# Performance work log

Measured on AMD Instinct MI355X. Metric: run time of the kernel, lower is better.

Reference implementation:

```python
import jax, jax.numpy as jnp
from jax import lax
import numpy as np

STRIDE = 16
PRE_NMS = 2000
POST_NMS = 300
NMS_THRESH = 0.7
MIN_SIZE = 16.0  # * img_scale (=1.0)
DN = ('NCHW', 'OIHW', 'NCHW')


def _anchor_base(base=16, ratios=(0.5, 1.0, 2.0), scales=(8, 16, 32)):
    py = px = base / 2.0
    ab = np.zeros((len(ratios) * len(scales), 4), np.float32)
    k = 0
    for r in ratios:
        for s in scales:
            h = base * s * np.sqrt(r)
            w = base * s * np.sqrt(1.0 / r)
            ab[k] = [py - h / 2, px - w / 2, py + h / 2, px + w / 2]
            k += 1
    return ab


def _all_anchors(H, W, img_h, img_w):
    base = _anchor_base()
    sy = np.arange(H, dtype=np.float32) * STRIDE
    sx = np.arange(W, dtype=np.float32) * STRIDE
    yy, xx = np.meshgrid(sy, sx, indexing='ij')
    shifts = np.stack([yy, xx, yy, xx], axis=-1).reshape(-1, 1, 4)
    anchors = (shifts + base[None]).reshape(-1, 4).astype(np.float32)  # (H*W*9, 4)
    valid = np.where((anchors[:, 0] >= 0) & (anchors[:, 1] >= 0) &
                     (anchors[:, 2] <= img_h) & (anchors[:, 3] <= img_w))[0]
    return anchors, valid


def _loc2bbox(anc, loc):
    # anc: (1,K,4), loc: (B,K,4); boxes as (y1,x1,y2,x2)
    h = anc[..., 2] - anc[..., 0]
    w = anc[..., 3] - anc[..., 1]
    cy = anc[..., 0] + 0.5 * h
    cx = anc[..., 1] + 0.5 * w
    ncy = loc[..., 0] * h + cy
    ncx = loc[..., 1] * w + cx
    nh = h * jnp.exp(loc[..., 2])
    nw = w * jnp.exp(loc[..., 3])
    return jnp.stack([ncy - 0.5 * nh, ncx - 0.5 * nw,
                      ncy + 0.5 * nh, ncx + 0.5 * nw], axis=-1)


def _nms(boxes, scores):
    # boxes: (N,4), scores: (N,) -> (POST_NMS,4) zero-padded rois
    areas = (boxes[:, 2] - boxes[:, 0]) * (boxes[:, 3] - boxes[:, 1])

    def step(s, _):
        i = jnp.argmax(s)
        ok = s[i] > -jnp.inf
        b = boxes[i]
        yy1 = jnp.maximum(b[0], boxes[:, 0])
        xx1 = jnp.maximum(b[1], boxes[:, 1])
        yy2 = jnp.minimum(b[2], boxes[:, 2])
        xx2 = jnp.minimum(b[3], boxes[:, 3])
        inter = jnp.maximum(yy2 - yy1, 0.0) * jnp.maximum(xx2 - xx1, 0.0)
        iou = inter / (areas[i] + areas - inter + 1e-9)
        s = jnp.where(iou > NMS_THRESH, -jnp.inf, s).at[i].set(-jnp.inf)
        return s, (i, ok)

    _, (idx, ok) = lax.scan(step, scores, None, length=POST_NMS)
    return boxes[idx] * ok[:, None].astype(boxes.dtype)


def _conv(x, w, b, padding):
    y = lax.conv_general_dilated(x, w, (1, 1), padding, dimension_numbers=DN)
    return y + b[None, :, None, None]


def setup_inputs():
    key = jax.random.key(0)
    k = jax.random.split(key, 4)
    B, C, H, W = 2, 512, 64, 64
    std = 0.01
    return {
        'feat': jax.random.normal(k[0], (B, C, H, W), jnp.float32),
        'share_w': jax.random.normal(k[1], (512, 512, 3, 3), jnp.float32) * std,
        'share_b': jnp.zeros((512,), jnp.float32),
        'cls_w': jax.random.normal(k[2], (18, 512, 1, 1), jnp.float32) * std,
        'cls_b': jnp.zeros((18,), jnp.float32),
        'reg_w': jax.random.normal(k[3], (36, 512, 1, 1), jnp.float32) * std,
        'reg_b': jnp.zeros((36,), jnp.float32),
        'img_h': 1024,
        'img_w': 1024,
    }


def reference(feat, share_w, share_b, cls_w, cls_b, reg_w, reg_b, img_h, img_w):
    B, _, H, W = feat.shape
    anchors_np, valid_np = _all_anchors(H, W, img_h, img_w)
    anchors = jnp.asarray(anchors_np)
    valid = jnp.asarray(valid_np)

    shared = jax.nn.relu(_conv(feat, share_w, share_b, 'SAME'))
    cls = _conv(shared, cls_w, cls_b, 'VALID')   # (B,18,H,W)
    reg = _conv(shared, reg_w, reg_b, 'VALID')   # (B,36,H,W)

    # permute(0,2,3,1).view(-1,2), gather valid anchors, softmax
    cls = cls.transpose(0, 2, 3, 1).reshape(B, -1, 2)[:, valid]   # (B,K,2)
    cls = jax.nn.softmax(cls, axis=-1)
    reg = reg.transpose(0, 2, 3, 1).reshape(B, -1, 4)[:, valid]   # (B,K,4)

    # proposal layer: decode, clip, min-size filter, top-k, NMS
    anc = anchors[valid][None]                                    # (1,K,4)
    boxes = _loc2bbox(anc, reg)                                   # (B,K,4)
    boxes = jnp.stack([jnp.clip(boxes[..., 0], 0.0, img_h),
                       jnp.clip(boxes[..., 1], 0.0, img_w),
                       jnp.clip(boxes[..., 2], 0.0, img_h),
                       jnp.clip(boxes[..., 3], 0.0, img_w)], axis=-1)
    hs = boxes[..., 2] - boxes[..., 0]
    ws = boxes[..., 3] - boxes[..., 1]
    scores = jnp.where((hs >= MIN_SIZE) & (ws >= MIN_SIZE), cls[..., 1], -jnp.inf)

    top_s, top_i = lax.top_k(scores, PRE_NMS)                     # (B,PRE_NMS)
    top_boxes = jnp.take_along_axis(boxes, top_i[..., None], axis=1)
    rois = jax.vmap(_nms)(top_boxes, top_s)                       # (B,POST_NMS,4)
    roi_list = rois.reshape(-1, 4)
    roi_id = jnp.repeat(jnp.arange(B, dtype=jnp.int32), POST_NMS)
    return cls, reg, roi_list, roi_id, anchors
```

## Files before the change

kernel.cpp:

```cpp
#include <hip/hip_runtime.h>
#include <math.h>

typedef unsigned int u32;
typedef unsigned long long u64;
typedef unsigned short ushort_t;

typedef __attribute__((ext_vector_type(8))) short short8;
typedef __attribute__((ext_vector_type(16))) float f32x16;

#define KANC 18376
#define PRE 2000
#define PREP 2048
#define POST 300

#define OUT_CLS 0
#define OUT_REG 73504
#define OUT_ROI 220512
#define OUT_RID 222912
#define OUT_ANC 223512

#define WS_NHWC   0u
#define WS_FT     16777216u
#define WS_W3     41943040u
#define WS_VPOS   56098816u
#define WS_BOXES  56246272u
#define WS_KEYS   56834304u
#define WS_TOPBOX 56981312u
#define WS_TOPKEY 57046848u
#define WS_MASK   57063232u

#define A_SPL2 7920

__device__ __forceinline__ ushort_t f2bf(float f) {
    u32 u = __float_as_uint(f);
    u32 r = (u + 0x7FFFu + ((u >> 16) & 1u)) >> 16;
    return (ushort_t)r;
}
__device__ __forceinline__ float bf2f(ushort_t h) {
    return __uint_as_float(((u32)h) << 16);
}
__device__ __forceinline__ u32 pack3(float v0, float v1, ushort_t* m0, ushort_t* m1,
                                     ushort_t* l0, ushort_t* l1) {
    ushort_t h0 = f2bf(v0);
    float r = v0 - bf2f(h0);
    *m0 = f2bf(r);
    *l0 = f2bf(r - bf2f(*m0));
    ushort_t h1 = f2bf(v1);
    float r1 = v1 - bf2f(h1);
    *m1 = f2bf(r1);
    *l1 = f2bf(r1 - bf2f(*m1));
    return (u32)h0 | ((u32)h1 << 16);
}

__device__ __forceinline__ void anchor_base(int t, float& y1, float& x1, float& y2, float& x2) {
    const double SQ[3] = {0.7071067811865476, 1.0, 1.4142135623730951};
    const double SC[3] = {8.0, 16.0, 32.0};
    int ri = t / 3, si = t % 3;
    double h = 16.0 * SC[si] * SQ[ri];
    double w = 16.0 * SC[si] * SQ[2 - ri];
    y1 = (float)(8.0 - h * 0.5);
    x1 = (float)(8.0 - w * 0.5);
    y2 = (float)(8.0 + h * 0.5);
    x2 = (float)(8.0 + w * 0.5);
}

__global__ __launch_bounds__(256) void t12_pre(const float* __restrict__ feat,
                                               const float* __restrict__ w,
                                               ushort_t* __restrict__ ft,
                                               ushort_t* __restrict__ w3,
                                               float* __restrict__ nhwc) {
    __shared__ float lds[8 * 577];
    int tid = threadIdx.x;
    int bid = blockIdx.x;
    if (bid < 1024) {
        float4 z4 = make_float4(0.f, 0.f, 0.f, 0.f);
        float4* nz = (float4*)nhwc + (size_t)bid * 1024;
        for (int i = tid; i < 1024; i += 256) nz[i] = z4;

        int by = bid >> 3;
        int b = by >> 6, y = by & 63;
        int ci0 = (bid & 7) * 64;
        for (int it = 0; it < 16; it++) {
            int idx = it * 256 + tid;
            int ci = idx >> 6, x = idx & 63;
            lds[ci * 65 + x] = feat[((size_t)(b * 512 + ci0 + ci) * 64 + y) * 64 + x];
        }
        __syncthreads();
        const size_t spl = (size_t)2 * 64 * 64 * 512;
        u32* ft32 = (u32*)ft;
        for (int it = 0; it < 8; it++) {
            int idx = it * 256 + tid;
            int x = idx >> 5, cp = idx & 31;
            float v0 = lds[(2 * cp) * 65 + x];
            float v1 = lds[(2 * cp + 1) * 65 + x];
            ushort_t m0, m1, l0, l1;
            u32 hi = pack3(v0, v1, &m0, &m1, &l0, &l1);
            size_t base = ((size_t)(b * 64 + y) * 64 + x) * 512 + ci0 + 2 * cp;
            ft32[base >> 1] = hi;
            ft32[(base + spl) >> 1] = (u32)m0 | ((u32)m1 << 16);
            ft32[(base + 2 * spl) >> 1] = (u32)l0 | ((u32)l1 << 16);
        }
    } else {
        int b2 = bid - 1024;
        int cob = b2 >> 3;
        int cib = (b2 & 7) * 64;
        for (int s = tid; s < 4608; s += 256) {
            int co = s / 576, r = s - co * 576;
            lds[co * 577 + r] = w[((size_t)(cob * 8 + co) * 512 + cib) * 9 + r];
        }
        __syncthreads();
        const size_t spl = (size_t)9 * 512 * 512;
        u32* w32 = (u32*)w3;
        int co = tid >> 5, cp = tid & 31;
        for (int kk = 0; kk < 9; kk++) {
            float v0 = lds[co * 577 + (2 * cp) * 9 + kk];
            float v1 = lds[co * 577 + (2 * cp + 1) * 9 + kk];
            ushort_t m0, m1, l0, l1;
            u32 hi = pack3(v0, v1, &m0, &m1, &l0, &l1);
            size_t base = ((size_t)kk * 512 + cob * 8 + co) * 512 + cib + 2 * cp;
            w32[base >> 1] = hi;
            w32[(base + spl) >> 1] = (u32)m0 | ((u32)m1 << 16);
            w32[(base + 2 * spl) >> 1] = (u32)l0 | ((u32)l1 << 16);
        }
    }
}

__global__ __launch_bounds__(256, 3) void k1_conv(const ushort_t* __restrict__ ft,
                                                  const ushort_t* __restrict__ w3,
                                                  float* __restrict__ nhwc) {
    __shared__ ushort_t lds16[3 * A_SPL2];
    int tid = threadIdx.x;
    int bid = blockIdx.x;
    int nt = bid & 1;
    int kh = (bid >> 1) & 3;
    int mt = bid >> 3;
    int b = mt >> 6, y = mt & 63;
    int nb = nt << 8;
    int ct0 = kh << 2;

    int lane = tid & 63;
    int w = tid >> 6;
    int wn = w << 6;
    int nlane = lane & 31;
    int kgrp8 = (lane >> 5) * 8;

    const size_t FT_SPL = (size_t)2 * 64 * 64 * 512;
    const size_t W3_SPL = (size_t)9 * 512 * 512;

    int sx = tid >> 2;
    int sq = tid & 3;

    f32x16 acc[2][2];
#pragma unroll
    for (int mi = 0; mi < 2; mi++)
#pragma unroll
        for (int ni = 0; ni < 2; ni++)
#pragma unroll
            for (int r = 0; r < 16; r++) acc[mi][ni][r] = 0.0f;

    if (tid < 72) {
        int s = tid / 24, rem = tid % 24;
        int r = rem >> 3, rem2 = rem & 7;
        int side = rem2 >> 2, q = rem2 & 3;
        uint4 z = make_uint4(0, 0, 0, 0);
        *(uint4*)&lds16[s * A_SPL2 + (r * 66 + side * 65) * 40 + q * 8] = z;
    }

    uint4 pbA[9];
    auto loadA = [&](int ct) {
#pragma unroll
        for (int r = 0; r < 3; r++) {
            int yy = y - 1 + r;
            bool valid = (yy >= 0 && yy < 64);
            size_t rowbase = ((size_t)(b * 64 + (valid ? yy : 0)) * 64 + sx) * 512 + ct * 32 + sq * 8;
#pragma unroll
            for (int s = 0; s < 3; s++) {
                uint4 v = make_uint4(0, 0, 0, 0);
                if (valid) v = *(const uint4*)&ft[rowbase + (size_t)s * FT_SPL];
                pbA[r * 3 + s] = v;
            }
        }
    };
    auto writeA = [&]() {
#pragma unroll
        for (int r = 0; r < 3; r++)
#pragma unroll
            for (int s = 0; s < 3; s++)
                *(uint4*)&lds16[s * A_SPL2 + (r * 66 + sx + 1) * 40 + sq * 8] = pbA[r * 3 + s];
    };

    short8 breg[2][2][3];
    auto loadB = [&](int buf, int tap, int ks, int ct) {
#pragma unroll
        for (int ni = 0; ni < 2; ni++) {
            size_t cobase = ((size_t)(tap * 512 + nb + wn + ni * 32 + nlane)) * 512
                            + ct * 32 + ks * 16 + kgrp8;
#pragma unroll
            for (int s = 0; s < 3; s++)
                breg[buf][ni][s] = *(const short8*)&w3[(size_t)s * W3_SPL + cobase];
        }
    };

    loadA(ct0);
    loadB(0, 0, 0, ct0);

    for (int ct = ct0; ct < ct0 + 4; ct++) {
        __syncthreads();
        writeA();
        __syncthreads();
        if (ct + 1 < ct0 + 4) loadA(ct + 1);

#pragma unroll
        for (int u = 0; u < 18; u++) {
            int cur = u & 1, alt = cur ^ 1;
            if (u + 1 < 18) loadB(alt, (u + 1) >> 1, (u + 1) & 1, ct);
            else if (ct + 1 < ct0 + 4) loadB(alt, 0, 0, ct + 1);
            int tap = u >> 1, ks = u & 1;
            int ky = tap / 3, kx = tap - ky * 3;

            short8 af[3][2];
#pragma unroll
            for (int s = 0; s < 3; s++) {
#pragma unroll
                for (int mi = 0; mi < 2; mi++)
                    af[s][mi] = *(const short8*)&lds16[s * A_SPL2 +
                        (ky * 66 + mi * 32 + nlane + kx) * 40 + ks * 16 + kgrp8];
            }
#pragma unroll
            for (int t = 0; t < 6; t++) {
                const int sa_t[6] = {0, 0, 1, 0, 1, 2};
                const int sb_t[6] = {0, 1, 0, 2, 1, 0};
                int sa = sa_t[t], sb = sb_t[t];
#pragma unroll
                for (int mi = 0; mi < 2; mi++)
#pragma unroll
                    for (int ni = 0; ni < 2; ni++)
                        acc[mi][ni] = __builtin_amdgcn_mfma_f32_32x32x16_bf16(
                            af[sa][mi], breg[cur][ni][sb], acc[mi][ni], 0, 0, 0);
            }
        }
    }

#pragma unroll
    for (int mi = 0; mi < 2; mi++) {
#pragma unroll
        for (int ni = 0; ni < 2; ni++) {
            int co = nb + wn + ni * 32 + nlane;
#pragma unroll
            for (int r = 0; r < 16; r++) {
                int xx = mi * 32 + (r & 3) + 8 * (r >> 2) + 4 * (lane >> 5);
                atomicAdd(&nhwc[((size_t)(b * 64 + y) * 64 + xx) * 512 + co], acc[mi][ni][r]);
            }
        }
    }
}

__global__ __launch_bounds__(256) void k2_heads(const float* __restrict__ nhwc,
                                                const float* __restrict__ share_b,
                                                const float* __restrict__ cls_w,
                                                const float* __restrict__ cls_b,
                                                const float* __restrict__ reg_w,
                                                const float* __restrict__ reg_b,
                                                float* __restrict__ out,
                                                float* __restrict__ boxes_ws,
                                                u32* __restrict__ keys_ws,
                                                const int* d_imgh, const int* d_imgw) {
    int bid = blockIdx.x;
    int row = bid >> 1;
    int b = row >> 6, y = row & 63;
    int h = bid & 1;
    int p0 = h * 32;
    int tid = threadIdx.x;
    __shared__ float Al[32 * 68];
    __shared__ float Wl[64 * 64];
    __shared__ float Ob[54 * 32];
    int og = tid & 15, pg = tid >> 4;
    float acc[2][4];
#pragma unroll
    for (int pp = 0; pp < 2; pp++)
#pragma unroll
        for (int j = 0; j < 4; j++) acc[pp][j] = 0.0f;

    for (int cib = 0; cib < 512; cib += 64) {
        for (int s = tid; s < 2048; s += 256) {
            int kk = s & 63, pp = s >> 6;
            float v = nhwc[((size_t)(b * 64 + y) * 64 + p0 + pp) * 512 + cib + kk]
                      + share_b[cib + kk];
            Al[pp * 68 + kk] = fmaxf(v, 0.0f);
        }
        for (int s = tid; s < 64 * 64; s += 256) {
            int o = s >> 6, kk = s & 63;
            float wv = 0.0f;
            if (o < 18) wv = cls_w[o * 512 + cib + kk];
            else if (o < 54) wv = reg_w[(o - 18) * 512 + cib + kk];
            Wl[s] = wv;
        }
        __syncthreads();
        for (int kq = 0; kq < 16; kq++) {
            float4 a0 = *(const float4*)&Al[(pg * 2) * 68 + kq * 4];
            float4 a1 = *(const float4*)&Al[(pg * 2 + 1) * 68 + kq * 4];
#pragma unroll
            for (int j = 0; j < 4; j++) {
                float4 w4 = *(const float4*)&Wl[(og * 4 + j) * 64 + kq * 4];
                acc[0][j] += a0.x * w4.x + a0.y * w4.y + a0.z * w4.z + a0.w * w4.w;
                acc[1][j] += a1.x * w4.x + a1.y * w4.y + a1.z * w4.z + a1.w * w4.w;
            }
        }
        __syncthreads();
    }
#pragma unroll
    for (int pp = 0; pp < 2; pp++)
#pragma unroll
        for (int j = 0; j < 4; j++) {
            int o = og * 4 + j;
            if (o < 54) {
                float bvv = (o < 18) ? cls_b[o] : reg_b[o - 18];
                Ob[o * 32 + pg * 2 + pp] = acc[pp][j] + bvv;
            }
        }
    __syncthreads();
    float imgh = (float)d_imgh[0], imgw = (float)d_imgw[0];
    for (int task = tid; task < 288; task += 256) {
        int ta = task >> 5, p2 = task & 31;
        int x = p0 + p2;
        int a_idx = (y * 64 + x) * 9 + ta;
        int j = 0;
        bool myvalid = false;
#pragma unroll
        for (int tt = 0; tt < 9; tt++) {
            float c0, c1, c2, c3;
            anchor_base(tt, c0, c1, c2, c3);
            int ylo = (int)((-c0) / 16.0f) + 1;
            int yhi = (int)((imgh - c2) / 16.0f);
            int xlo = (int)((-c1) / 16.0f) + 1;
            int xhi = (int)((imgw - c3) / 16.0f);
            ylo = max(ylo, 0); yhi = min(yhi, 63);
            xlo = max(xlo, 0); xhi = min(xhi, 63);
            int Wt  = max(xhi - xlo + 1, 0);
            int nry = max(yhi - ylo + 1, 0);
            int rb  = min(max(y - ylo, 0), nry);
            bool vy = (y >= ylo) && (y <= yhi);
            int cb  = vy ? min(max(x - xlo, 0), Wt) : 0;
            bool val = vy && (x >= xlo) && (x <= xhi);
            j += rb * Wt + cb + ((tt < ta && val) ? 1 : 0);
            if (tt == ta) {
                myvalid = val;
                float4 o4;
                o4.x = c0 + 16.0f * y;
                o4.y = c1 + 16.0f * x;
                o4.z = c2 + 16.0f * y;
                o4.w = c3 + 16.0f * x;
                *(float4*)&out[OUT_ANC + a_idx * 4] = o4;
            }
        }
        if (!myvalid) continue;
        float c0 = Ob[(2 * ta) * 32 + p2], c1 = Ob[(2 * ta + 1) * 32 + p2];
        float m = fmaxf(c0, c1);
        float e0 = expf(c0 - m), e1 = expf(c1 - m);
        float sden = e0 + e1;
        float p0v = e0 / sden, p1v = e1 / sden;
        out[OUT_CLS + (size_t)(b * KANC + j) * 2 + 0] = p0v;
        out[OUT_CLS + (size_t)(b * KANC + j) * 2 + 1] = p1v;
        float l0 = Ob[(18 + 4 * ta + 0) * 32 + p2];
        float l1 = Ob[(18 + 4 * ta + 1) * 32 + p2];
        float l2 = Ob[(18 + 4 * ta + 2) * 32 + p2];
        float l3 = Ob[(18 + 4 * ta + 3) * 32 + p2];
        out[OUT_REG + (size_t)(b * KANC + j) * 4 + 0] = l0;
        out[OUT_REG + (size_t)(b * KANC + j) * 4 + 1] = l1;
        out[OUT_REG + (size_t)(b * KANC + j) * 4 + 2] = l2;
        out[OUT_REG + (size_t)(b * KANC + j) * 4 + 3] = l3;
        float b0, b1, b2, b3; anchor_base(ta, b0, b1, b2, b3);
        float ay1 = b0 + 16.0f * y, ax1 = b1 + 16.0f * x;
        float ay2 = b2 + 16.0f * y, ax2 = b3 + 16.0f * x;
        float hh = ay2 - ay1, wdt = ax2 - ax1;
        float cy = ay1 + 0.5f * hh, cx = ax1 + 0.5f * wdt;
        float ncy = l0 * hh + cy, ncx = l1 * wdt + cx;
        float nh = hh * expf(l2), nw = wdt * expf(l3);
        float by1 = fminf(fmaxf(ncy - 0.5f * nh, 0.0f), imgh);
        float bx1 = fminf(fmaxf(ncx - 0.5f * nw, 0.0f), imgw);
        float by2 = fminf(fmaxf(ncy + 0.5f * nh, 0.0f), imgh);
        float bx2 = fminf(fmaxf(ncx + 0.5f * nw, 0.0f), imgw);
        boxes_ws[(size_t)(b * KANC + j) * 4 + 0] = by1;
        boxes_ws[(size_t)(b * KANC + j) * 4 + 1] = bx1;
        boxes_ws[(size_t)(b * KANC + j) * 4 + 2] = by2;
        boxes_ws[(size_t)(b * KANC + j) * 4 + 3] = bx2;
        float hs = by2 - by1, wsz = bx2 - bx1;
        u32 key = 0;
        if (hs >= 16.0f && wsz >= 16.0f) key = __float_as_uint(p1v) + 1u;
        keys_ws[b * KANC + j] = key;
    }
}

__device__ __forceinline__ void suffix_scan(u32* suf, const u32* hist, int N, int tid) {
    for (int i = tid; i < N; i += 1024) suf[i] = hist[i];
    if (tid == 0) suf[N] = 0;
    __syncthreads();
    for (int off = 1; off < N; off <<= 1) {
        u32 add0 = 0, add1 = 0;
        int i0 = tid, i1 = tid + 1024;
        if (i0 < N) add0 = (i0 + off < N) ? suf[i0 + off] : 0;
        if (i1 < N) add1 = (i1 + off < N) ? suf[i1 + off] : 0;
        __syncthreads();
        if (i0 < N) suf[i0] += add0;
        if (i1 < N) suf[i1] += add1;
        __syncthreads();
    }
}

__global__ __launch_bounds__(1024) void k3_select(const u32* __restrict__ keys_ws,
                                                  const float* __restrict__ boxes_ws,
                                                  u32* __restrict__ topkey,
                                                  float* __restrict__ topbox) {
    int b = blockIdx.x, tid = threadIdx.x;
    const u32* keys = keys_ws + (size_t)b * KANC;
    __shared__ u32 hist[2048];
    __shared__ u32 suf[2049];
    __shared__ int Ps;
    __shared__ int cnt;
    __shared__ u64 sbuf[2048];

    for (int i = tid; i < 2048; i += 1024) hist[i] = 0;
    __syncthreads();
    for (int i = tid; i < KANC; i += 1024) atomicAdd(&hist[keys[i] >> 20], 1u);
    __syncthreads();
    suffix_scan(suf, hist, 2048, tid);
    if (tid == 0) Ps = 0;
    __syncthreads();
    for (int i = tid; i < 2048; i += 1024)
        if (suf[i] >= (u32)PRE && suf[i + 1] < (u32)PRE) Ps = i;
    __syncthreads();
    u32 P1 = (u32)Ps;
    u32 quota2 = (u32)PRE - suf[P1 + 1];
    __syncthreads();

    for (int i = tid; i < 1024; i += 1024) hist[i] = 0;
    __syncthreads();
    for (int i = tid; i < KANC; i += 1024) {
        u32 k = keys[i];
        if ((k >> 20) == P1) atomicAdd(&hist[(k >> 10) & 1023u], 1u);
    }
    __syncthreads();
    suffix_scan(suf, hist, 1024, tid);
    if (tid == 0) Ps = 0;
    __syncthreads();
    for (int i = tid; i < 1024; i += 1024)
        if (suf[i] >= quota2 && suf[i + 1] < quota2) Ps = i;
    __syncthreads();
    u32 P2 = (u32)Ps;
    u32 quota3 = quota2 - suf[P2 + 1];
    __syncthreads();

    u32 pref = (P1 << 10) | P2;
    for (int i = tid; i < 1024; i += 1024) hist[i] = 0;
    __syncthreads();
    for (int i = tid; i < KANC; i += 1024) {
        u32 k = keys[i];
        if ((k >> 10) == pref) atomicAdd(&hist[k & 1023u], 1u);
    }
    __syncthreads();
    suffix_scan(suf, hist, 1024, tid);
    if (tid == 0) Ps = 0;
    __syncthreads();
    for (int i = tid; i < 1024; i += 1024)
        if (suf[i] >= quota3 && suf[i + 1] < quota3) Ps = i;
    __syncthreads();
    u32 P3 = (u32)Ps;
    u32 T = (P1 << 20) | (P2 << 10) | P3;
    u32 Tm = (T < 1u) ? 1u : T;

    for (int i = tid; i < 2048; i += 1024) sbuf[i] = 0ull;
    if (tid == 0) cnt = 0;
    __syncthreads();
    for (int i = tid; i < KANC; i += 1024) {
        u32 k = keys[i];
        if (k >= Tm) {
            int pos = atomicAdd(&cnt, 1);
            if (pos < 2048)
                sbuf[pos] = ((u64)k << 32) | (u64)(0xFFFFFFFFu - (u32)i);
        }
    }
    __syncthreads();

    for (int k2 = 2; k2 <= 2048; k2 <<= 1) {
        for (int j2 = k2 >> 1; j2 > 0; j2 >>= 1) {
            for (int i = tid; i < 2048; i += 1024) {
                int ixj = i ^ j2;
                if (ixj > i) {
                    u64 va = sbuf[i], vb = sbuf[ixj];
                    bool descRegion = ((i & k2) == 0);
                    if (descRegion ? (va < vb) : (va > vb)) {
                        sbuf[i] = vb; sbuf[ixj] = va;
                    }
                }
            }
            __syncthreads();
        }
    }

    for (int i = tid; i < PREP; i += 1024) {
        u64 v = sbuf[i];
        u32 kk = (u32)(v >> 32);
        u32 j = 0xFFFFFFFFu - (u32)(v & 0xFFFFFFFFull);
        bool good = (i < PRE) && (kk != 0);
        topkey[b * PREP + i] = good ? kk : 0;
        float4 bx = make_float4(0.0f, 0.0f, 0.0f, 0.0f);
        if (good) bx = *(const float4*)&boxes_ws[(size_t)(b * KANC + j) * 4];
        *(float4*)&topbox[(size_t)(b * PREP + i) * 4] = bx;
    }
}

__global__ __launch_bounds__(64) void k4_mask(const float* __restrict__ topbox,
                                              u64* __restrict__ mask) {
    int jb = blockIdx.x, ib = blockIdx.y, b = blockIdx.z;
    int lane = threadIdx.x;
    float4 bi = *(const float4*)&topbox[(size_t)(b * PREP + ib * 64 + lane) * 4];
    float4 bj = *(const float4*)&topbox[(size_t)(b * PREP + jb * 64 + lane) * 4];
    float ai = (bi.z - bi.x) * (bi.w - bi.y);
    float aj = (bj.z - bj.x) * (bj.w - bj.y);
    u64 word = 0;
    for (int ii = 0; ii < 64; ii++) {
        float y1 = __shfl(bi.x, ii), x1 = __shfl(bi.y, ii);
        float y2 = __shfl(bi.z, ii), x2 = __shfl(bi.w, ii);
        float aii = __shfl(ai, ii);
        float yy1 = fmaxf(y1, bj.x), xx1 = fmaxf(x1, bj.y);
        float yy2 = fminf(y2, bj.z), xx2 = fminf(x2, bj.w);
        float inter = fmaxf(yy2 - yy1, 0.0f) * fmaxf(xx2 - xx1, 0.0f);
        float iou = inter / (aii + aj - inter + 1e-9f);
        u64 bal = __ballot(iou > 0.7f);
        if (lane == ii) word = bal;
    }
    mask[(size_t)(b * PREP + ib * 64 + lane) * 32 + jb] = word;
}

__global__ __launch_bounds__(64) void k5_nms(const u32* __restrict__ topkey,
                                             const float* __restrict__ topbox,
                                             const u64* __restrict__ mask,
                                             float* __restrict__ out) {
    int b = blockIdx.x;
    int lane = threadIdx.x;
    __shared__ int kept[POST];

    u64 validw = 0;
    for (int it = 0; it < 32; it++) {
        u64 wv = __ballot(topkey[b * PREP + it * 64 + lane] != 0);
        if (lane == it) validw = wv;
    }

    const u64* mb = mask + (size_t)b * PREP * 32;
    u64 remv = 0;
    const int CH = 16;
    u64 bufA[CH], bufB[CH];
    auto loadRows = [&](u64* buf, int base) {
#pragma unroll
        for (int k = 0; k < CH; k++)
            buf[k] = (lane < 32) ? mb[(size_t)(base + k) * 32 + lane] : 0ull;
    };
    int nk = 0;
    auto process = [&](u64* buf, int base) {
        int wi = base >> 6, sh = base & 63;
        u64 supw = __shfl(remv, wi);
        u64 valw = __shfl(validw, wi);
        u32 cand = (u32)(((~supw & valw) >> sh) & 0xFFFFull);
        while (cand) {
            int k = __builtin_ctz(cand);
            cand &= cand - 1;
            int i = base + k;
            remv |= buf[k];
            u64 rw = __shfl(buf[k], wi);
            cand &= ~((u32)((rw >> sh) & 0xFFFFull));
            if (lane == 0) kept[nk] = i;
            nk++;
            if (nk == POST) break;
        }
    };

    loadRows(bufA, 0);
    for (int base = 0; base < PRE && nk < POST; base += 2 * CH) {
        loadRows(bufB, base + CH);
        process(bufA, base);
        if (nk < POST && base + CH < PRE) {
            if (base + 2 * CH < PRE) loadRows(bufA, base + 2 * CH);
            process(bufB, base + CH);
        }
    }
    __syncthreads();
    for (int s = lane; s < POST; s += 64) {
        float4 bx = make_float4(0.0f, 0.0f, 0.0f, 0.0f);
        if (s < nk) bx = *(const float4*)&topbox[(size_t)(b * PREP + kept[s]) * 4];
        *(float4*)&out[OUT_ROI + (size_t)(b * POST + s) * 4] = bx;
        out[OUT_RID + b * POST + s] = (float)b;
    }
}

extern "C" void kernel_launch(void* const* d_in, const int* in_sizes, int n_in,
                              void* d_out, int out_size, void* d_ws, size_t ws_size,
                              hipStream_t stream) {
    (void)in_sizes; (void)n_in; (void)out_size; (void)ws_size;
    const float* feat    = (const float*)d_in[0];
    const float* share_w = (const float*)d_in[1];
    const float* share_b = (const float*)d_in[2];
    const float* cls_w   = (const float*)d_in[3];
    const float* cls_b   = (const float*)d_in[4];
    const float* reg_w   = (const float*)d_in[5];
    const float* reg_b   = (const float*)d_in[6];
    const int*   imgh    = (const int*)d_in[7];
    const int*   imgw    = (const int*)d_in[8];
    float* out = (float*)d_out;
    char* ws = (char*)d_ws;
    float*     nhwc   = (float*)(ws + WS_NHWC);
    ushort_t*  ft     = (ushort_t*)(ws + WS_FT);
    ushort_t*  w3     = (ushort_t*)(ws + WS_W3);
    float*     boxes  = (float*)(ws + WS_BOXES);
    u32*       keys   = (u32*)(ws + WS_KEYS);
    float*     topbox = (float*)(ws + WS_TOPBOX);
    u32*       topkey = (u32*)(ws + WS_TOPKEY);
    u64*       maskp  = (u64*)(ws + WS_MASK);

    t12_pre<<<1536, 256, 0, stream>>>(feat, share_w, ft, w3, nhwc);
    k1_conv<<<1024, 256, 0, stream>>>(ft, w3, nhwc);
    k2_heads<<<256, 256, 0, stream>>>(nhwc, share_b, cls_w, cls_b, reg_w, reg_b,
                                      out, boxes, keys, imgh, imgw);
    k3_select<<<2, 1024, 0, stream>>>(keys, boxes, topkey, topbox);
    k4_mask<<<dim3(32, 32, 2), 64, 0, stream>>>(topbox, maskp);
    k5_nms<<<2, 64, 0, stream>>>(topkey, topbox, maskp, out);
}
```

Baseline: 673.0 us.

## Halve conv split-K, restructure top-k radix select, skip lower-triangle NMS mask

The conv kernel now splits K two ways instead of four, so each block covers 8 channel tiles and half as many fp32 atomics reach the NHWC buffer; launch bounds drop to 2 waves per SIMD and the grid halves. The top-k select uses an 8-copy privatised 512-bin first histogram and 9/11/11-bit radix passes, and compacts candidates with a wave-level ballot so there is one atomic per wave. The NMS mask kernel skips IoU work for lower-triangle blocks and writes zeros there. The trade is less conv parallelism and lower occupancy in exchange for fewer atomics and less select and mask work.

```diff
diff --git a/kernel.cpp b/kernel.cpp
--- a/kernel.cpp
+++ b/kernel.cpp
@@ -125,18 +125,18 @@
     }
 }
 
-__global__ __launch_bounds__(256, 3) void k1_conv(const ushort_t* __restrict__ ft,
+__global__ __launch_bounds__(256, 2) void k1_conv(const ushort_t* __restrict__ ft,
                                                   const ushort_t* __restrict__ w3,
                                                   float* __restrict__ nhwc) {
     __shared__ ushort_t lds16[3 * A_SPL2];
     int tid = threadIdx.x;
     int bid = blockIdx.x;
-    int nt = bid & 1;
-    int kh = (bid >> 1) & 3;
-    int mt = bid >> 3;
+    int nt = (bid >> 1) & 1;
+    int kh = (bid >> 2) & 1;
+    int mt = ((bid >> 3) << 1) | (bid & 1);
     int b = mt >> 6, y = mt & 63;
     int nb = nt << 8;
-    int ct0 = kh << 2;
+    int ct0 = kh * 8;
 
     int lane = tid & 63;
     int w = tid >> 6;
@@ -150,13 +150,12 @@
     int sx = tid >> 2;
     int sq = tid & 3;
 
-    f32x16 acc[2][2];
-#pragma unroll
-    for (int mi = 0; mi < 2; mi++)
-#pragma unroll
-        for (int ni = 0; ni < 2; ni++)
-#pragma unroll
-            for (int r = 0; r < 16; r++) acc[mi][ni][r] = 0.0f;
+    f32x16 acc[2];
+    f32x16 acc2[2];
+#pragma unroll
+    for (int ni = 0; ni < 2; ni++)
+#pragma unroll
+        for (int r = 0; r < 16; r++) { acc[ni][r] = 0.0f; acc2[ni][r] = 0.0f; }
 
     if (tid < 72) {
         int s = tid / 24, rem = tid % 24;
@@ -204,17 +203,17 @@
     loadA(ct0);
     loadB(0, 0, 0, ct0);
 
-    for (int ct = ct0; ct < ct0 + 4; ct++) {
+    for (int ct = ct0; ct < ct0 + 8; ct++) {
         __syncthreads();
         writeA();
         __syncthreads();
-        if (ct + 1 < ct0 + 4) loadA(ct + 1);
+        if (ct + 1 < ct0 + 8) loadA(ct + 1);
 
 #pragma unroll
         for (int u = 0; u < 18; u++) {
             int cur = u & 1, alt = cur ^ 1;
             if (u + 1 < 18) loadB(alt, (u + 1) >> 1, (u + 1) & 1, ct);
-            else if (ct + 1 < ct0 + 4) loadB(alt, 0, 0, ct + 1);
+            else if (ct + 1 < ct0 + 8) loadB(alt, 0, 0, ct + 1);
             int tap = u >> 1, ks = u & 1;
             int ky = tap / 3, kx = tap - ky * 3;
 
@@ -232,25 +231,24 @@
                 const int sb_t[6] = {0, 1, 0, 2, 1, 0};
                 int sa = sa_t[t], sb = sb_t[t];
 #pragma unroll
-                for (int mi = 0; mi < 2; mi++)
-#pragma unroll
-                    for (int ni = 0; ni < 2; ni++)
-                        acc[mi][ni] = __builtin_amdgcn_mfma_f32_32x32x16_bf16(
-                            af[sa][mi], breg[cur][ni][sb], acc[mi][ni], 0, 0, 0);
-            }
-        }
-    }
-
-#pragma unroll
-    for (int mi = 0; mi < 2; mi++) {
-#pragma unroll
-        for (int ni = 0; ni < 2; ni++) {
-            int co = nb + wn + ni * 32 + nlane;
-#pragma unroll
-            for (int r = 0; r < 16; r++) {
-                int xx = mi * 32 + (r & 3) + 8 * (r >> 2) + 4 * (lane >> 5);
-                atomicAdd(&nhwc[((size_t)(b * 64 + y) * 64 + xx) * 512 + co], acc[mi][ni][r]);
-            }
+                for (int ni = 0; ni < 2; ni++) {
+                    acc[ni]  = __builtin_amdgcn_mfma_f32_32x32x16_bf16(
+                        af[sa][0], breg[cur][ni][sb], acc[ni], 0, 0, 0);
+                    acc2[ni] = __builtin_amdgcn_mfma_f32_32x32x16_bf16(
+                        af[sa][1], breg[cur][ni][sb], acc2[ni], 0, 0, 0);
+                }
+            }
+        }
+    }
+
+#pragma unroll
+    for (int ni = 0; ni < 2; ni++) {
+        int co = nb + wn + ni * 32 + nlane;
+#pragma unroll
+        for (int r = 0; r < 16; r++) {
+            int xx = (r & 3) + 8 * (r >> 2) + 4 * (lane >> 5);
+            atomicAdd(&nhwc[((size_t)(b * 64 + y) * 64 + xx) * 512 + co], acc[ni][r]);
+            atomicAdd(&nhwc[((size_t)(b * 64 + y) * 64 + 32 + xx) * 512 + co], acc2[ni][r]);
         }
     }
 }
@@ -413,70 +411,89 @@
                                                   float* __restrict__ topbox) {
     int b = blockIdx.x, tid = threadIdx.x;
     const u32* keys = keys_ws + (size_t)b * KANC;
+    __shared__ u64 sbuf[2048];
     __shared__ u32 hist[2048];
     __shared__ u32 suf[2049];
     __shared__ int Ps;
     __shared__ int cnt;
-    __shared__ u64 sbuf[2048];
+
+    u32* hist_p = (u32*)sbuf;
+    int cpy = tid >> 7;
+    for (int i = tid; i < 4096; i += 1024) hist_p[i] = 0;
+    __syncthreads();
+    for (int i = tid; i < KANC; i += 1024) atomicAdd(&hist_p[cpy * 512 + (keys[i] >> 22)], 1u);
+    __syncthreads();
+    for (int bin = tid; bin < 512; bin += 1024) {
+        u32 s = 0;
+#pragma unroll
+        for (int c = 0; c < 8; c++) s += hist_p[c * 512 + bin];
+        hist[bin] = s;
+    }
+    __syncthreads();
+    suffix_scan(suf, hist, 512, tid);
+    if (tid == 0) Ps = 0;
+    __syncthreads();
+    for (int i = tid; i < 512; i += 1024)
+        if (suf[i] >= (u32)PRE && suf[i + 1] < (u32)PRE) Ps = i;
+    __syncthreads();
+    u32 P1 = (u32)Ps;
+    u32 quota2 = (u32)PRE - suf[P1 + 1];
+    __syncthreads();
 
     for (int i = tid; i < 2048; i += 1024) hist[i] = 0;
     __syncthreads();
-    for (int i = tid; i < KANC; i += 1024) atomicAdd(&hist[keys[i] >> 20], 1u);
+    for (int i = tid; i < KANC; i += 1024) {
+        u32 k = keys[i];
+        if ((k >> 22) == P1) atomicAdd(&hist[(k >> 11) & 2047u], 1u);
+    }
     __syncthreads();
     suffix_scan(suf, hist, 2048, tid);
     if (tid == 0) Ps = 0;
     __syncthreads();
     for (int i = tid; i < 2048; i += 1024)
-        if (suf[i] >= (u32)PRE && suf[i + 1] < (u32)PRE) Ps = i;
-    __syncthreads();
-    u32 P1 = (u32)Ps;
-    u32 quota2 = (u32)PRE - suf[P1 + 1];
-    __syncthreads();
-
-    for (int i = tid; i < 1024; i += 1024) hist[i] = 0;
+        if (suf[i] >= quota2 && suf[i + 1] < quota2) Ps = i;
+    __syncthreads();
+    u32 P2 = (u32)Ps;
+    u32 quota3 = quota2 - suf[P2 + 1];
+    __syncthreads();
+
+    u32 pref = (P1 << 11) | P2;
+    for (int i = tid; i < 2048; i += 1024) hist[i] = 0;
     __syncthreads();
     for (int i = tid; i < KANC; i += 1024) {
         u32 k = keys[i];
-        if ((k >> 20) == P1) atomicAdd(&hist[(k >> 10) & 1023u], 1u);
-    }
-    __syncthreads();
-    suffix_scan(suf, hist, 1024, tid);
+        if ((k >> 11) == pref) atomicAdd(&hist[k & 2047u], 1u);
+    }
+    __syncthreads();
+    suffix_scan(suf, hist, 2048, tid);
     if (tid == 0) Ps = 0;
     __syncthreads();
-    for (int i = tid; i < 1024; i += 1024)
-        if (suf[i] >= quota2 && suf[i + 1] < quota2) Ps = i;
-    __syncthreads();
-    u32 P2 = (u32)Ps;
-    u32 quota3 = quota2 - suf[P2 + 1];
-    __syncthreads();
-
-    u32 pref = (P1 << 10) | P2;
-    for (int i = tid; i < 1024; i += 1024) hist[i] = 0;
-    __syncthreads();
-    for (int i = tid; i < KANC; i += 1024) {
-        u32 k = keys[i];
-        if ((k >> 10) == pref) atomicAdd(&hist[k & 1023u], 1u);
-    }
-    __syncthreads();
-    suffix_scan(suf, hist, 1024, tid);
-    if (tid == 0) Ps = 0;
-    __syncthreads();
-    for (int i = tid; i < 1024; i += 1024)
+    for (int i = tid; i < 2048; i += 1024)
         if (suf[i] >= quota3 && suf[i + 1] < quota3) Ps = i;
     __syncthreads();
     u32 P3 = (u32)Ps;
-    u32 T = (P1 << 20) | (P2 << 10) | P3;
+    u32 T = (P1 << 22) | (P2 << 11) | P3;
     u32 Tm = (T < 1u) ? 1u : T;
 
+    __syncthreads();
     for (int i = tid; i < 2048; i += 1024) sbuf[i] = 0ull;
     if (tid == 0) cnt = 0;
     __syncthreads();
-    for (int i = tid; i < KANC; i += 1024) {
-        u32 k = keys[i];
-        if (k >= Tm) {
-            int pos = atomicAdd(&cnt, 1);
-            if (pos < 2048)
-                sbuf[pos] = ((u64)k << 32) | (u64)(0xFFFFFFFFu - (u32)i);
+    int lane = tid & 63;
+    for (int i = tid; i < KANC + 1023; i += 1024) {
+        u32 k = (i < KANC) ? keys[i] : 0u;
+        bool p = (i < KANC) && (k >= Tm);
+        u64 m = __ballot(p);
+        if (m) {
+            int ldr = __ffsll((unsigned long long)m) - 1;
+            int base = 0;
+            if (lane == ldr) base = atomicAdd(&cnt, __popcll(m));
+            base = __shfl(base, ldr);
+            if (p) {
+                int pos = base + __popcll(m & ((1ull << lane) - 1ull));
+                if (pos < 2048)
+                    sbuf[pos] = ((u64)k << 32) | (u64)(0xFFFFFFFFu - (u32)i);
+            }
         }
     }
     __syncthreads();
@@ -513,6 +530,10 @@
                                               u64* __restrict__ mask) {
     int jb = blockIdx.x, ib = blockIdx.y, b = blockIdx.z;
     int lane = threadIdx.x;
+    if (jb < ib) {
+        mask[(size_t)(b * PREP + ib * 64 + lane) * 32 + jb] = 0ull;
+        return;
+    }
     float4 bi = *(const float4*)&topbox[(size_t)(b * PREP + ib * 64 + lane) * 4];
     float4 bj = *(const float4*)&topbox[(size_t)(b * PREP + jb * 64 + lane) * 4];
     float ai = (bi.z - bi.x) * (bi.w - bi.y);
@@ -617,7 +638,7 @@
     u64*       maskp  = (u64*)(ws + WS_MASK);
 
     t12_pre<<<1536, 256, 0, stream>>>(feat, share_w, ft, w3, nhwc);
-    k1_conv<<<1024, 256, 0, stream>>>(ft, w3, nhwc);
+    k1_conv<<<512, 256, 0, stream>>>(ft, w3, nhwc);
     k2_heads<<<256, 256, 0, stream>>>(nhwc, share_b, cls_w, cls_b, reg_w, reg_b,
                                       out, boxes, keys, imgh, imgw);
     k3_select<<<2, 1024, 0, stream>>>(keys, boxes, topkey, topbox);
```

Result: faster. 622.7 us, median of 2 (-7.5%).
